# Performance work log

Measured on AMD Instinct MI355X. Metric: run time of the kernel, lower is better.

## Reference

```python
import jax, jax.numpy as jnp
import numpy as np

DIM = 1024
NUM_HEADS = 16
DPH = DIM // NUM_HEADS
B, S = 4, 2048
LN_EPS = 1e-5


def layer_norm(x, g, b):
    mu = jnp.mean(x, axis=-1, keepdims=True)
    var = jnp.mean((x - mu) ** 2, axis=-1, keepdims=True)
    return (x - mu) * jax.lax.rsqrt(var + LN_EPS) * g + b


def setup_inputs() -> dict:
    key = jax.random.key(0)
    ks = jax.random.split(key, 10)
    sd = 0.02
    return {
        "x": jax.random.normal(ks[0], (B, S, DIM), dtype=jnp.float32),
        "Wq": jax.random.normal(ks[1], (DIM, DIM), dtype=jnp.float32) * sd,
        "Wk": jax.random.normal(ks[2], (DIM, DIM), dtype=jnp.float32) * sd,
        "Wv": jax.random.normal(ks[3], (DIM, DIM), dtype=jnp.float32) * sd,
        "bq": jnp.zeros((DIM,), dtype=jnp.float32),
        "bk": jnp.zeros((DIM,), dtype=jnp.float32),
        "bv": jnp.zeros((DIM,), dtype=jnp.float32),
        "ln1_g": jnp.ones((DIM,), dtype=jnp.float32),
        "ln1_b": jnp.zeros((DIM,), dtype=jnp.float32),
        "W1": jax.random.normal(ks[4], (DIM, 4 * DIM), dtype=jnp.float32) * sd,
        "b1": jnp.zeros((4 * DIM,), dtype=jnp.float32),
        "W2": jax.random.normal(ks[5], (4 * DIM, DIM), dtype=jnp.float32) * sd,
        "b2": jnp.zeros((DIM,), dtype=jnp.float32),
        "ln2_g": jnp.ones((DIM,), dtype=jnp.float32),
        "ln2_b": jnp.zeros((DIM,), dtype=jnp.float32),
    }


def reference(x, Wq, Wk, Wv, bq, bk, bv, ln1_g, ln1_b, W1, b1, W2, b2, ln2_g, ln2_b):
    b, s, d = x.shape
    # QKV projections (heads are independent linears -> one fused GEMM each)
    q = (x @ Wq + bq).reshape(b, s, NUM_HEADS, DPH)
    k = (x @ Wk + bk).reshape(b, s, NUM_HEADS, DPH)
    v = (x @ Wv + bv).reshape(b, s, NUM_HEADS, DPH)
    # Faithful quirk: module scales by 1/sqrt(dph) twice => 1/dph total
    scores = jnp.einsum("bqhd,bkhd->bhqk", q, k) / DPH
    causal = jnp.tril(jnp.ones((s, s), dtype=bool))
    scores = jnp.where(causal, scores, -1e9)
    attn = jax.nn.softmax(scores, axis=-1)
    out_attn = jnp.einsum("bhqk,bkhd->bqhd", attn, v).reshape(b, s, d)
    # Add & Norm 1 (no output projection in original)
    h = layer_norm(out_attn + x, ln1_g, ln1_b)
    # Feed-forward (dropout is identity at eval)
    ffn = jax.nn.relu(h @ W1 + b1) @ W2 + b2
    # Add & Norm 2
    return layer_norm(ffn + h, ln2_g, ln2_b)
```

## Files before the change

### kernel.cpp

```cpp
#include <hip/hip_runtime.h>
#include <hip/hip_bf16.h>

typedef __bf16 bf16_t;
typedef __bf16 bf16x8 __attribute__((ext_vector_type(8)));
typedef __bf16 bf16x4 __attribute__((ext_vector_type(4)));
typedef float  floatx4 __attribute__((ext_vector_type(4)));

#define DIM    1024
#define S_LEN  2048
#define NHEAD  16

template <typename T>
__device__ __forceinline__ bf16x8 load8bf(const T* src) {
  if constexpr (sizeof(T) == 2) {
    return *reinterpret_cast<const bf16x8*>(src);
  } else {
    floatx4 f0 = *reinterpret_cast<const floatx4*>(src);
    floatx4 f1 = *reinterpret_cast<const floatx4*>(src + 4);
    bf16x8 h;
    h[0] = (bf16_t)f0[0]; h[1] = (bf16_t)f0[1];
    h[2] = (bf16_t)f0[2]; h[3] = (bf16_t)f0[3];
    h[4] = (bf16_t)f1[0]; h[5] = (bf16_t)f1[1];
    h[6] = (bf16_t)f1[2]; h[7] = (bf16_t)f1[3];
    return h;
  }
}

__global__ __launch_bounds__(256) void convT3(
    const float* __restrict__ in0, int ldi0, bf16_t* __restrict__ out0,
    const float* __restrict__ in1, int ldi1, bf16_t* __restrict__ out1,
    const float* __restrict__ in2, int ldi2, bf16_t* __restrict__ out2,
    int ldo) {
  __shared__ bf16_t tile[32][33];
  const int z = blockIdx.z;
  const float* in = (z == 0) ? in0 : ((z == 1) ? in1 : in2);
  bf16_t* out = (z == 0) ? out0 : ((z == 1) ? out1 : out2);
  int ldi = (z == 0) ? ldi0 : ((z == 1) ? ldi1 : ldi2);
  int tx = threadIdx.x, ty = threadIdx.y;
  int n0 = blockIdx.x * 32, k0 = blockIdx.y * 32;
#pragma unroll
  for (int i = 0; i < 4; ++i)
    tile[ty + 8 * i][tx] = (bf16_t)in[(size_t)(k0 + ty + 8 * i) * ldi + n0 + tx];
  __syncthreads();
#pragma unroll
  for (int i = 0; i < 4; ++i)
    out[(size_t)(n0 + ty + 8 * i) * ldo + k0 + tx] = tile[tx][ty + 8 * i];
}

#define BM 128
#define BN 128
#define BK 32
#define LSTR 40

template <typename TA>
__global__ __launch_bounds__(256) void gemm_abt(
    const TA* __restrict__ A, int lda,
    const bf16_t* __restrict__ Bt, int zBRow,
    bf16_t* __restrict__ C, int ldc, int zCOff,
    const float* __restrict__ bias0, const float* __restrict__ bias1,
    const float* __restrict__ bias2,
    int K, int relu, int accum) {
  __shared__ bf16_t As[BM * LSTR];
  __shared__ bf16_t Bs[BN * LSTR];
  const int z = blockIdx.z;
  const float* bias = (z == 0) ? bias0 : ((z == 1) ? bias1 : bias2);
  const bf16_t* Bz = Bt + (size_t)z * zBRow * K;
  C += (size_t)z * zCOff;

  const int tid  = threadIdx.x;
  const int lane = tid & 63;
  const int wave = tid >> 6;
  const int wr   = wave >> 1;
  const int wc   = wave & 1;
  const int quad = lane >> 4;
  const int l15  = lane & 15;
  const int m0   = blockIdx.y * BM;
  const int n0   = blockIdx.x * BN;

  floatx4 acc[4][4];
#pragma unroll
  for (int i = 0; i < 4; ++i)
#pragma unroll
    for (int j = 0; j < 4; ++j) acc[i][j] = (floatx4)(0.0f);

  const int kIters = K / BK;
  for (int kt = 0; kt < kIters; ++kt) {
#pragma unroll
    for (int p = 0; p < 2; ++p) {
      int id  = p * 256 + tid;
      int row = id >> 2;
      int c8  = (id & 3) * 8;
      *reinterpret_cast<bf16x8*>(&As[row * LSTR + c8]) =
          load8bf(A + (size_t)(m0 + row) * lda + kt * BK + c8);
      *reinterpret_cast<bf16x8*>(&Bs[row * LSTR + c8]) =
          *reinterpret_cast<const bf16x8*>(Bz + (size_t)(n0 + row) * K + kt * BK + c8);
    }
    __syncthreads();

    bf16x8 a[4], b[4];
#pragma unroll
    for (int i = 0; i < 4; ++i)
      a[i] = *reinterpret_cast<const bf16x8*>(&As[(wr * 64 + i * 16 + l15) * LSTR + quad * 8]);
#pragma unroll
    for (int j = 0; j < 4; ++j)
      b[j] = *reinterpret_cast<const bf16x8*>(&Bs[(wc * 64 + j * 16 + l15) * LSTR + quad * 8]);
#pragma unroll
    for (int i = 0; i < 4; ++i)
#pragma unroll
      for (int j = 0; j < 4; ++j)
        acc[i][j] = __builtin_amdgcn_mfma_f32_16x16x32_bf16(a[i], b[j], acc[i][j], 0, 0, 0);
    __syncthreads();
  }

#pragma unroll
  for (int j = 0; j < 4; ++j) {
    int gn = n0 + wc * 64 + j * 16 + l15;
    float bv = bias ? bias[gn] : 0.0f;
#pragma unroll
    for (int i = 0; i < 4; ++i) {
      int gm = m0 + wr * 64 + i * 16 + quad * 4;
#pragma unroll
      for (int r = 0; r < 4; ++r) {
        float v = acc[i][j][r] + bv;
        if (relu) v = fmaxf(v, 0.0f);
        size_t idx = (size_t)(gm + r) * ldc + gn;
        if (accum) v += (float)C[idx];
        C[idx] = (bf16_t)v;
      }
    }
  }
}

__global__ __launch_bounds__(256) void transpose_v(const bf16_t* __restrict__ in,
                                                   bf16_t* __restrict__ outp) {
  __shared__ bf16_t tile[32][33];
  int tx = threadIdx.x, ty = threadIdx.y;
  int s0 = blockIdx.x * 32, d0 = blockIdx.y * 32, bh = blockIdx.z;
  int z = bh >> 4, h = bh & 15;
  const bf16_t* src = in + (size_t)z * S_LEN * 3072 + 2048 + h * 64;
#pragma unroll
  for (int i = 0; i < 4; ++i)
    tile[ty + 8 * i][tx] = src[(size_t)(s0 + ty + 8 * i) * 3072 + d0 + tx];
  __syncthreads();
  bf16_t* dst = outp + (size_t)bh * 64 * S_LEN;
#pragma unroll
  for (int i = 0; i < 4; ++i)
    dst[(size_t)(d0 + ty + 8 * i) * S_LEN + s0 + tx] = tile[tx][ty + 8 * i];
}

#define TQ  64
#define TK  64
#define AST 72

__global__ __launch_bounds__(256, 2) void attn_mfma2(
    const bf16_t* __restrict__ qkv, const bf16_t* __restrict__ vt,
    float* __restrict__ out) {
  __shared__ bf16_t QsPs[TQ * AST];
  __shared__ bf16_t Ks[TK * AST];
  __shared__ bf16_t Vs[TK * AST];

  const int tid  = threadIdx.x;
  const int lane = tid & 63;
  const int w    = tid >> 6;
  const int quad = lane >> 4;
  const int l15  = lane & 15;
  const int pi   = blockIdx.x;
  const int h    = blockIdx.y;
  const int z    = blockIdx.z;
  const int qb[2] = {pi, 31 - pi};
  const bf16_t* qkv_b = qkv + (size_t)z * S_LEN * 3072;
  const bf16_t* vt_bh = vt + ((size_t)z * NHEAD + h) * 64 * S_LEN;
  float* out_b = out + (size_t)z * S_LEN * DIM;

  bf16x8 aq[2][2];
  for (int tile = 0; tile < 2; ++tile) {
    if (tile) __syncthreads();
    const int qg0 = qb[tile] * TQ;
#pragma unroll
    for (int p = 0; p < 2; ++p) {
      int id  = p * 256 + tid;
      int row = id >> 3;
      int c8  = (id & 7) * 8;
      bf16x8 v = *reinterpret_cast<const bf16x8*>(
          qkv_b + (size_t)(qg0 + row) * 3072 + h * 64 + c8);
      bf16x8 o;
#pragma unroll
      for (int e = 0; e < 8; ++e) o[e] = (bf16_t)((float)v[e] * 0.015625f);
      *reinterpret_cast<bf16x8*>(&QsPs[row * AST + c8]) = o;
    }
    __syncthreads();
#pragma unroll
    for (int ks = 0; ks < 2; ++ks)
      aq[tile][ks] = *reinterpret_cast<const bf16x8*>(
          &QsPs[(w * 16 + l15) * AST + ks * 32 + quad * 8]);
  }

  float m_run[2][4], l_run[2][4];
  floatx4 O[2][4];
#pragma unroll
  for (int t = 0; t < 2; ++t)
#pragma unroll
    for (int r = 0; r < 4; ++r) {
      m_run[t][r] = -1e30f; l_run[t][r] = 0.0f;
    }
#pragma unroll
  for (int t = 0; t < 2; ++t)
#pragma unroll
    for (int dt = 0; dt < 4; ++dt) O[t][dt] = (floatx4)(0.0f);

  const int ktEnd = qb[1] + 1;
  for (int kt = 0; kt < ktEnd; ++kt) {
    __syncthreads();
#pragma unroll
    for (int p = 0; p < 2; ++p) {
      int id  = p * 256 + tid;
      int row = id >> 3;
      int c8  = (id & 7) * 8;
      *reinterpret_cast<bf16x8*>(&Ks[row * AST + c8]) =
          *reinterpret_cast<const bf16x8*>(
              qkv_b + (size_t)(kt * TK + row) * 3072 + 1024 + h * 64 + c8);
      *reinterpret_cast<bf16x8*>(&Vs[row * AST + c8]) =
          *reinterpret_cast<const bf16x8*>(
              vt_bh + (size_t)row * S_LEN + kt * TK + c8);
    }
    __syncthreads();

    bf16x8 bk[4][2], bv[4][2];
#pragma unroll
    for (int i = 0; i < 4; ++i)
#pragma unroll
      for (int ks = 0; ks < 2; ++ks) {
        bk[i][ks] = *reinterpret_cast<const bf16x8*>(
            &Ks[(i * 16 + l15) * AST + ks * 32 + quad * 8]);
        bv[i][ks] = *reinterpret_cast<const bf16x8*>(
            &Vs[(i * 16 + l15) * AST + ks * 32 + quad * 8]);
      }

#pragma unroll
    for (int tile = 0; tile < 2; ++tile) {
      const int qtb = qb[tile] * TQ + w * 16;
      if (kt * TK > qtb + 15) continue;

      floatx4 s[4];
#pragma unroll
      for (int ktl = 0; ktl < 4; ++ktl) {
        s[ktl] = __builtin_amdgcn_mfma_f32_16x16x32_bf16(
            aq[tile][0], bk[ktl][0], (floatx4)(0.0f), 0, 0, 0);
        s[ktl] = __builtin_amdgcn_mfma_f32_16x16x32_bf16(
            aq[tile][1], bk[ktl][1], s[ktl], 0, 0, 0);
      }
      if (kt * TK + TK - 1 > qtb) {
#pragma unroll
        for (int ktl = 0; ktl < 4; ++ktl) {
          int gk = kt * TK + ktl * 16 + l15;
#pragma unroll
          for (int r = 0; r < 4; ++r) {
            int gq = qtb + quad * 4 + r;
            if (gk > gq) s[ktl][r] = -1e30f;
          }
        }
      }
      float lsum[4], alpha[4];
#pragma unroll
      for (int r = 0; r < 4; ++r) {
        float mv = fmaxf(fmaxf(s[0][r], s[1][r]), fmaxf(s[2][r], s[3][r]));
#pragma unroll
        for (int off = 1; off < 16; off <<= 1)
          mv = fmaxf(mv, __shfl_xor(mv, off));
        float mn = fmaxf(m_run[tile][r], mv);
        alpha[r] = __expf(m_run[tile][r] - mn);
        m_run[tile][r] = mn;
        lsum[r] = 0.0f;
      }
#pragma unroll
      for (int ktl = 0; ktl < 4; ++ktl)
#pragma unroll
        for (int r = 0; r < 4; ++r) {
          float p = __expf(s[ktl][r] - m_run[tile][r]);
          s[ktl][r] = p;
          lsum[r] += p;
        }
#pragma unroll
      for (int r = 0; r < 4; ++r) {
#pragma unroll
        for (int off = 1; off < 16; off <<= 1)
          lsum[r] += __shfl_xor(lsum[r], off);
        l_run[tile][r] = l_run[tile][r] * alpha[r] + lsum[r];
      }
#pragma unroll
      for (int dt = 0; dt < 4; ++dt)
#pragma unroll
        for (int r = 0; r < 4; ++r) O[tile][dt][r] *= alpha[r];
#pragma unroll
      for (int ktl = 0; ktl < 4; ++ktl)
#pragma unroll
        for (int r = 0; r < 4; ++r)
          QsPs[(w * 16 + quad * 4 + r) * AST + ktl * 16 + l15] =
              (bf16_t)s[ktl][r];

      bf16x8 ap0 = *reinterpret_cast<const bf16x8*>(
          &QsPs[(w * 16 + l15) * AST + quad * 8]);
      bf16x8 ap1 = *reinterpret_cast<const bf16x8*>(
          &QsPs[(w * 16 + l15) * AST + 32 + quad * 8]);
#pragma unroll
      for (int dt = 0; dt < 4; ++dt) {
        O[tile][dt] = __builtin_amdgcn_mfma_f32_16x16x32_bf16(
            ap0, bv[dt][0], O[tile][dt], 0, 0, 0);
        O[tile][dt] = __builtin_amdgcn_mfma_f32_16x16x32_bf16(
            ap1, bv[dt][1], O[tile][dt], 0, 0, 0);
      }
    }
  }

#pragma unroll
  for (int tile = 0; tile < 2; ++tile) {
    const int qg0 = qb[tile] * TQ;
    float inv[4];
#pragma unroll
    for (int r = 0; r < 4; ++r) inv[r] = 1.0f / l_run[tile][r];
#pragma unroll
    for (int dt = 0; dt < 4; ++dt)
#pragma unroll
      for (int r = 0; r < 4; ++r)
        out_b[(size_t)(qg0 + w * 16 + quad * 4 + r) * DIM +
              h * 64 + dt * 16 + l15] = O[tile][dt][r] * inv[r];
  }
}

template <typename TA>
__global__ __launch_bounds__(256) void add_ln_k(const TA* a,
                                                const float* b,
                                                const float* __restrict__ g,
                                                const float* __restrict__ be,
                                                float* out) {
  const int row = blockIdx.x;
  const int t   = threadIdx.x;
  const size_t base = (size_t)row * DIM;

  float x[4];
  {
    floatx4 bv = *reinterpret_cast<const floatx4*>(b + base + t * 4);
    if constexpr (sizeof(TA) == 2) {
      bf16x4 av = *reinterpret_cast<const bf16x4*>(a + base + t * 4);
#pragma unroll
      for (int i = 0; i < 4; ++i) x[i] = (float)av[i] + bv[i];
    } else {
      floatx4 av = *reinterpret_cast<const floatx4*>(a + base + t * 4);
#pragma unroll
      for (int i = 0; i < 4; ++i) x[i] = av[i] + bv[i];
    }
  }
  float s1 = 0.0f, s2 = 0.0f;
#pragma unroll
  for (int i = 0; i < 4; ++i) { s1 += x[i]; s2 += x[i] * x[i]; }
#pragma unroll
  for (int off = 32; off; off >>= 1) {
    s1 += __shfl_xor(s1, off);
    s2 += __shfl_xor(s2, off);
  }
  __shared__ float ls1[4], ls2[4];
  if ((t & 63) == 0) { ls1[t >> 6] = s1; ls2[t >> 6] = s2; }
  __syncthreads();
  float S1 = ls1[0] + ls1[1] + ls1[2] + ls1[3];
  float S2 = ls2[0] + ls2[1] + ls2[2] + ls2[3];
  float mu  = S1 * (1.0f / DIM);
  float var = S2 * (1.0f / DIM) - mu * mu;
  float rs  = rsqrtf(var + 1e-5f);
#pragma unroll
  for (int i = 0; i < 4; ++i) {
    int c = t * 4 + i;
    out[base + c] = (x[i] - mu) * rs * g[c] + be[c];
  }
}

extern "C" void kernel_launch(void* const* d_in, const int* in_sizes, int n_in,
                              void* d_out, int out_size, void* d_ws, size_t ws_size,
                              hipStream_t stream) {
  const float* x   = (const float*)d_in[0];
  const float* Wq  = (const float*)d_in[1];
  const float* Wk  = (const float*)d_in[2];
  const float* Wv  = (const float*)d_in[3];
  const float* bq  = (const float*)d_in[4];
  const float* bk  = (const float*)d_in[5];
  const float* bv  = (const float*)d_in[6];
  const float* g1  = (const float*)d_in[7];
  const float* be1 = (const float*)d_in[8];
  const float* W1  = (const float*)d_in[9];
  const float* b1  = (const float*)d_in[10];
  const float* W2  = (const float*)d_in[11];
  const float* b2  = (const float*)d_in[12];
  const float* g2  = (const float*)d_in[13];
  const float* be2 = (const float*)d_in[14];
  float* out = (float*)d_out;
  char*  ws  = (char*)d_ws;

  bf16_t* WqkvT = (bf16_t*)(ws);
  bf16_t* qkv2  = (bf16_t*)(ws + 6291456);
  bf16_t* vt    = (bf16_t*)(ws + 31457280);
  bf16_t* W1Tq  = (bf16_t*)(ws);
  bf16_t* W2Tq  = (bf16_t*)(ws + 2097152);
  bf16_t* mid   = (bf16_t*)(ws + 4194304);
  bf16_t* ffnO  = (bf16_t*)(ws + 20971520);

  dim3 tb(32, 8);
  convT3<<<dim3(32, 32, 3), tb, 0, stream>>>(
      Wq, 1024, WqkvT, Wk, 1024, WqkvT + 1048576, Wv, 1024, WqkvT + 2097152, 1024);

  for (int p = 0; p < 2; ++p) {
    const float* xp   = x   + (size_t)p * 2 * S_LEN * DIM;
    float*       outp = out + (size_t)p * 2 * S_LEN * DIM;
    gemm_abt<float><<<dim3(8, 32, 3), 256, 0, stream>>>(
        xp, 1024, WqkvT, 1024, qkv2, 3072, 1024, bq, bk, bv, 1024, 0, 0);
    transpose_v<<<dim3(64, 2, 32), tb, 0, stream>>>(qkv2, vt);
    attn_mfma2<<<dim3(16, 16, 2), 256, 0, stream>>>(qkv2, vt, outp);
  }
  add_ln_k<float><<<8192, 256, 0, stream>>>(out, x, g1, be1, out);

  for (int q = 0; q < 4; ++q) {
    convT3<<<dim3(32, 32, 2), tb, 0, stream>>>(
        W1 + q * 1024, 4096, W1Tq,
        W2 + (size_t)q * 1024 * 1024, 1024, W2Tq,
        nullptr, 0, nullptr, 1024);
    gemm_abt<float><<<dim3(8, 64, 1), 256, 0, stream>>>(
        out, 1024, W1Tq, 0, mid, 1024, 0, b1 + q * 1024, nullptr, nullptr,
        1024, 1, 0);
    gemm_abt<bf16_t><<<dim3(8, 64, 1), 256, 0, stream>>>(
        mid, 1024, W2Tq, 0, ffnO, 1024, 0, (q == 0) ? b2 : nullptr, nullptr,
        nullptr, 1024, 0, (q > 0) ? 1 : 0);
  }
  add_ln_k<bf16_t><<<8192, 256, 0, stream>>>(ffnO, out, g2, be2, out);
}
```

Measured before the change: 769.0 us.

## Split attention to one query tile per block with register-prefetched K/V

The attention kernel now processes a single 64-row query tile per block, with longest-first ordering via reversed blockIdx, instead of pairing tiles pi and 31-pi. The grid doubles and launch bounds rise to 4 blocks per CU. K/V tiles for the next step are prefetched into registers while the current tile is computed, and B-operands are read from LDS on demand rather than held in registers. This aims to overlap global loads with compute and raise occupancy, at the cost of losing the paired load balancing and adding an extra sync per step.

Result: slower. 837.0 us (+8.8%).

```diff
diff --git a/kernel.cpp b/kernel.cpp
--- a/kernel.cpp
+++ b/kernel.cpp
@@ -152,7 +152,9 @@
 #define TK  64
 #define AST 72
 
-__global__ __launch_bounds__(256, 2) void attn_mfma2(
+struct KVregs { bf16x8 k[2]; bf16x8 v[2]; };
+
+__global__ __launch_bounds__(256, 4) void attn_mfma2(
     const bf16_t* __restrict__ qkv, const bf16_t* __restrict__ vt,
     float* __restrict__ out) {
   __shared__ bf16_t QsPs[TQ * AST];
@@ -164,167 +166,164 @@
   const int w    = tid >> 6;
   const int quad = lane >> 4;
   const int l15  = lane & 15;
-  const int pi   = blockIdx.x;
+  const int qt   = 31 - blockIdx.x;
   const int h    = blockIdx.y;
   const int z    = blockIdx.z;
-  const int qb[2] = {pi, 31 - pi};
   const bf16_t* qkv_b = qkv + (size_t)z * S_LEN * 3072;
   const bf16_t* vt_bh = vt + ((size_t)z * NHEAD + h) * 64 * S_LEN;
   float* out_b = out + (size_t)z * S_LEN * DIM;
-
-  bf16x8 aq[2][2];
-  for (int tile = 0; tile < 2; ++tile) {
-    if (tile) __syncthreads();
-    const int qg0 = qb[tile] * TQ;
+  const int qg0 = qt * TQ;
+  const int qtb = qg0 + w * 16;
+
+#pragma unroll
+  for (int p = 0; p < 2; ++p) {
+    int id  = p * 256 + tid;
+    int row = id >> 3;
+    int c8  = (id & 7) * 8;
+    bf16x8 v = *reinterpret_cast<const bf16x8*>(
+        qkv_b + (size_t)(qg0 + row) * 3072 + h * 64 + c8);
+    bf16x8 o;
+#pragma unroll
+    for (int e = 0; e < 8; ++e) o[e] = (bf16_t)((float)v[e] * 0.015625f);
+    *reinterpret_cast<bf16x8*>(&QsPs[row * AST + c8]) = o;
+  }
+  __syncthreads();
+  bf16x8 aq[2];
+#pragma unroll
+  for (int ks = 0; ks < 2; ++ks)
+    aq[ks] = *reinterpret_cast<const bf16x8*>(
+        &QsPs[(w * 16 + l15) * AST + ks * 32 + quad * 8]);
+
+  float m_run[4], l_run[4];
+  floatx4 O[4];
+#pragma unroll
+  for (int r = 0; r < 4; ++r) { m_run[r] = -1e30f; l_run[r] = 0.0f; }
+#pragma unroll
+  for (int dt = 0; dt < 4; ++dt) O[dt] = (floatx4)(0.0f);
+
+  const int ktEnd = qt + 1;
+
+  auto kv_load = [&](KVregs& r, int kt) {
 #pragma unroll
     for (int p = 0; p < 2; ++p) {
       int id  = p * 256 + tid;
       int row = id >> 3;
       int c8  = (id & 7) * 8;
-      bf16x8 v = *reinterpret_cast<const bf16x8*>(
-          qkv_b + (size_t)(qg0 + row) * 3072 + h * 64 + c8);
-      bf16x8 o;
-#pragma unroll
-      for (int e = 0; e < 8; ++e) o[e] = (bf16_t)((float)v[e] * 0.015625f);
-      *reinterpret_cast<bf16x8*>(&QsPs[row * AST + c8]) = o;
-    }
-    __syncthreads();
-#pragma unroll
-    for (int ks = 0; ks < 2; ++ks)
-      aq[tile][ks] = *reinterpret_cast<const bf16x8*>(
-          &QsPs[(w * 16 + l15) * AST + ks * 32 + quad * 8]);
-  }
-
-  float m_run[2][4], l_run[2][4];
-  floatx4 O[2][4];
-#pragma unroll
-  for (int t = 0; t < 2; ++t)
-#pragma unroll
-    for (int r = 0; r < 4; ++r) {
-      m_run[t][r] = -1e30f; l_run[t][r] = 0.0f;
-    }
-#pragma unroll
-  for (int t = 0; t < 2; ++t)
-#pragma unroll
-    for (int dt = 0; dt < 4; ++dt) O[t][dt] = (floatx4)(0.0f);
-
-  const int ktEnd = qb[1] + 1;
-  for (int kt = 0; kt < ktEnd; ++kt) {
-    __syncthreads();
+      r.k[p] = *reinterpret_cast<const bf16x8*>(
+          qkv_b + (size_t)(kt * TK + row) * 3072 + 1024 + h * 64 + c8);
+      r.v[p] = *reinterpret_cast<const bf16x8*>(
+          vt_bh + (size_t)row * S_LEN + kt * TK + c8);
+    }
+  };
+  auto kv_write = [&](KVregs& r) {
 #pragma unroll
     for (int p = 0; p < 2; ++p) {
       int id  = p * 256 + tid;
       int row = id >> 3;
       int c8  = (id & 7) * 8;
-      *reinterpret_cast<bf16x8*>(&Ks[row * AST + c8]) =
-          *reinterpret_cast<const bf16x8*>(
-              qkv_b + (size_t)(kt * TK + row) * 3072 + 1024 + h * 64 + c8);
-      *reinterpret_cast<bf16x8*>(&Vs[row * AST + c8]) =
-          *reinterpret_cast<const bf16x8*>(
-              vt_bh + (size_t)row * S_LEN + kt * TK + c8);
-    }
+      *reinterpret_cast<bf16x8*>(&Ks[row * AST + c8]) = r.k[p];
+      *reinterpret_cast<bf16x8*>(&Vs[row * AST + c8]) = r.v[p];
+    }
+  };
+
+  auto step = [&](int kt, KVregs& cur, KVregs& nxt) {
+    if (kt + 1 < ktEnd) kv_load(nxt, kt + 1);
     __syncthreads();
-
-    bf16x8 bk[4][2], bv[4][2];
-#pragma unroll
-    for (int i = 0; i < 4; ++i)
-#pragma unroll
-      for (int ks = 0; ks < 2; ++ks) {
-        bk[i][ks] = *reinterpret_cast<const bf16x8*>(
-            &Ks[(i * 16 + l15) * AST + ks * 32 + quad * 8]);
-        bv[i][ks] = *reinterpret_cast<const bf16x8*>(
-            &Vs[(i * 16 + l15) * AST + ks * 32 + quad * 8]);
-      }
-
-#pragma unroll
-    for (int tile = 0; tile < 2; ++tile) {
-      const int qtb = qb[tile] * TQ + w * 16;
-      if (kt * TK > qtb + 15) continue;
-
-      floatx4 s[4];
+    kv_write(cur);
+    __syncthreads();
+
+    floatx4 s[4];
+#pragma unroll
+    for (int ktl = 0; ktl < 4; ++ktl) {
+      bf16x8 k0 = *reinterpret_cast<const bf16x8*>(
+          &Ks[(ktl * 16 + l15) * AST + quad * 8]);
+      bf16x8 k1 = *reinterpret_cast<const bf16x8*>(
+          &Ks[(ktl * 16 + l15) * AST + 32 + quad * 8]);
+      s[ktl] = __builtin_amdgcn_mfma_f32_16x16x32_bf16(
+          aq[0], k0, (floatx4)(0.0f), 0, 0, 0);
+      s[ktl] = __builtin_amdgcn_mfma_f32_16x16x32_bf16(
+          aq[1], k1, s[ktl], 0, 0, 0);
+    }
+    if (kt == qt) {
 #pragma unroll
       for (int ktl = 0; ktl < 4; ++ktl) {
-        s[ktl] = __builtin_amdgcn_mfma_f32_16x16x32_bf16(
-            aq[tile][0], bk[ktl][0], (floatx4)(0.0f), 0, 0, 0);
-        s[ktl] = __builtin_amdgcn_mfma_f32_16x16x32_bf16(
-            aq[tile][1], bk[ktl][1], s[ktl], 0, 0, 0);
-      }
-      if (kt * TK + TK - 1 > qtb) {
-#pragma unroll
-        for (int ktl = 0; ktl < 4; ++ktl) {
-          int gk = kt * TK + ktl * 16 + l15;
-#pragma unroll
-          for (int r = 0; r < 4; ++r) {
-            int gq = qtb + quad * 4 + r;
-            if (gk > gq) s[ktl][r] = -1e30f;
-          }
+        int gk = kt * TK + ktl * 16 + l15;
+#pragma unroll
+        for (int r = 0; r < 4; ++r) {
+          int gq = qtb + quad * 4 + r;
+          if (gk > gq) s[ktl][r] = -1e30f;
         }
       }
-      float lsum[4], alpha[4];
+    }
+    float lsum[4], alpha[4];
+#pragma unroll
+    for (int r = 0; r < 4; ++r) {
+      float mv = fmaxf(fmaxf(s[0][r], s[1][r]), fmaxf(s[2][r], s[3][r]));
+#pragma unroll
+      for (int off = 1; off < 16; off <<= 1)
+        mv = fmaxf(mv, __shfl_xor(mv, off));
+      float mn = fmaxf(m_run[r], mv);
+      alpha[r] = __expf(m_run[r] - mn);
+      m_run[r] = mn;
+      lsum[r] = 0.0f;
+    }
+#pragma unroll
+    for (int ktl = 0; ktl < 4; ++ktl)
 #pragma unroll
       for (int r = 0; r < 4; ++r) {
-        float mv = fmaxf(fmaxf(s[0][r], s[1][r]), fmaxf(s[2][r], s[3][r]));
-#pragma unroll
-        for (int off = 1; off < 16; off <<= 1)
-          mv = fmaxf(mv, __shfl_xor(mv, off));
-        float mn = fmaxf(m_run[tile][r], mv);
-        alpha[r] = __expf(m_run[tile][r] - mn);
-        m_run[tile][r] = mn;
-        lsum[r] = 0.0f;
+        float p = __expf(s[ktl][r] - m_run[r]);
+        s[ktl][r] = p;
+        lsum[r] += p;
       }
 #pragma unroll
-      for (int ktl = 0; ktl < 4; ++ktl)
-#pragma unroll
-        for (int r = 0; r < 4; ++r) {
-          float p = __expf(s[ktl][r] - m_run[tile][r]);
-          s[ktl][r] = p;
-          lsum[r] += p;
-        }
-#pragma unroll
-      for (int r = 0; r < 4; ++r) {
-#pragma unroll
-        for (int off = 1; off < 16; off <<= 1)
-          lsum[r] += __shfl_xor(lsum[r], off);
-        l_run[tile][r] = l_run[tile][r] * alpha[r] + lsum[r];
-      }
-#pragma unroll
-      for (int dt = 0; dt < 4; ++dt)
-#pragma unroll
-        for (int r = 0; r < 4; ++r) O[tile][dt][r] *= alpha[r];
-#pragma unroll
-      for (int ktl = 0; ktl < 4; ++ktl)
-#pragma unroll
-        for (int r = 0; r < 4; ++r)
-          QsPs[(w * 16 + quad * 4 + r) * AST + ktl * 16 + l15] =
-              (bf16_t)s[ktl][r];
-
-      bf16x8 ap0 = *reinterpret_cast<const bf16x8*>(
-          &QsPs[(w * 16 + l15) * AST + quad * 8]);
-      bf16x8 ap1 = *reinterpret_cast<const bf16x8*>(
-          &QsPs[(w * 16 + l15) * AST + 32 + quad * 8]);
-#pragma unroll
-      for (int dt = 0; dt < 4; ++dt) {
-        O[tile][dt] = __builtin_amdgcn_mfma_f32_16x16x32_bf16(
-            ap0, bv[dt][0], O[tile][dt], 0, 0, 0);
-        O[tile][dt] = __builtin_amdgcn_mfma_f32_16x16x32_bf16(
-            ap1, bv[dt][1], O[tile][dt], 0, 0, 0);
-      }
-    }
-  }
-
-#pragma unroll
-  for (int tile = 0; tile < 2; ++tile) {
-    const int qg0 = qb[tile] * TQ;
-    float inv[4];
-#pragma unroll
-    for (int r = 0; r < 4; ++r) inv[r] = 1.0f / l_run[tile][r];
+    for (int r = 0; r < 4; ++r) {
+#pragma unroll
+      for (int off = 1; off < 16; off <<= 1)
+        lsum[r] += __shfl_xor(lsum[r], off);
+      l_run[r] = l_run[r] * alpha[r] + lsum[r];
+    }
 #pragma unroll
     for (int dt = 0; dt < 4; ++dt)
 #pragma unroll
+      for (int r = 0; r < 4; ++r) O[dt][r] *= alpha[r];
+#pragma unroll
+    for (int ktl = 0; ktl < 4; ++ktl)
+#pragma unroll
       for (int r = 0; r < 4; ++r)
-        out_b[(size_t)(qg0 + w * 16 + quad * 4 + r) * DIM +
-              h * 64 + dt * 16 + l15] = O[tile][dt][r] * inv[r];
-  }
+        QsPs[(w * 16 + quad * 4 + r) * AST + ktl * 16 + l15] =
+            (bf16_t)s[ktl][r];
+
+    bf16x8 ap0 = *reinterpret_cast<const bf16x8*>(
+        &QsPs[(w * 16 + l15) * AST + quad * 8]);
+    bf16x8 ap1 = *reinterpret_cast<const bf16x8*>(
+        &QsPs[(w * 16 + l15) * AST + 32 + quad * 8]);
+#pragma unroll
+    for (int dt = 0; dt < 4; ++dt) {
+      bf16x8 v0 = *reinterpret_cast<const bf16x8*>(
+          &Vs[(dt * 16 + l15) * AST + quad * 8]);
+      bf16x8 v1 = *reinterpret_cast<const bf16x8*>(
+          &Vs[(dt * 16 + l15) * AST + 32 + quad * 8]);
+      O[dt] = __builtin_amdgcn_mfma_f32_16x16x32_bf16(ap0, v0, O[dt], 0, 0, 0);
+      O[dt] = __builtin_amdgcn_mfma_f32_16x16x32_bf16(ap1, v1, O[dt], 0, 0, 0);
+    }
+  };
+
+  KVregs A, B;
+  kv_load(A, 0);
+  for (int kt = 0; kt < ktEnd; kt += 2) {
+    step(kt, A, B);
+    if (kt + 1 < ktEnd) step(kt + 1, B, A);
+  }
+
+  float inv[4];
+#pragma unroll
+  for (int r = 0; r < 4; ++r) inv[r] = 1.0f / l_run[r];
+#pragma unroll
+  for (int dt = 0; dt < 4; ++dt)
+#pragma unroll
+    for (int r = 0; r < 4; ++r)
+      out_b[(size_t)(qg0 + w * 16 + quad * 4 + r) * DIM +
+            h * 64 + dt * 16 + l15] = O[dt][r] * inv[r];
 }
 
 template <typename TA>
@@ -412,7 +411,7 @@
     gemm_abt<float><<<dim3(8, 32, 3), 256, 0, stream>>>(
         xp, 1024, WqkvT, 1024, qkv2, 3072, 1024, bq, bk, bv, 1024, 0, 0);
     transpose_v<<<dim3(64, 2, 32), tb, 0, stream>>>(qkv2, vt);
-    attn_mfma2<<<dim3(16, 16, 2), 256, 0, stream>>>(qkv2, vt, outp);
+    attn_mfma2<<<dim3(32, 16, 2), 256, 0, stream>>>(qkv2, vt, outp);
   }
   add_ln_k<float><<<8192, 256, 0, stream>>>(out, x, g1, be1, out);
 
```
